# Performance work log

Measured on AMD Instinct MI355X. Metric: run time of the kernel, lower is better.

Reference implementation:

```python
import jax, jax.numpy as jnp
import numpy as np

N = 131072
L = 8
NPL = N // L          # nodes per topological level
DEG = 16              # fixed in-degree
D = 128               # hidden_dim
NEG_SLOPE = 0.01


def _mlp(x, w1, b1, w2, b2, w3, b3):
    # MLP(D, D/2, D/2, D) with LeakyReLU(0.01) between layers
    x = jax.nn.leaky_relu(x @ w1 + b1, NEG_SLOPE)
    x = jax.nn.leaky_relu(x @ w2 + b2, NEG_SLOPE)
    return x @ w3 + b3


def setup_inputs() -> dict:
    key = jax.random.key(0)
    ks = jax.random.split(key, 32)
    h = jax.random.normal(ks[0], (N, D), dtype=jnp.float32)
    # topological DAG: level i nodes pull from nodes in levels < i
    src_levels = []
    for i in range(1, L):
        src_levels.append(jax.random.randint(ks[i], (NPL, DEG), 0, i * NPL, dtype=jnp.int32))
    edge_src = jnp.stack(src_levels)                      # [L-1, NPL, DEG]
    edge_mask = jax.random.randint(ks[10], (L - 1, NPL, DEG), 0, 2, dtype=jnp.int32)
    H = D // 2
    s = 1.0 / np.sqrt(D)
    s2 = 1.0 / np.sqrt(H)

    def lin(k, i, o, sc):
        return jax.random.uniform(k, (i, o), jnp.float32, -sc, sc)

    params = {}
    for j, name in enumerate(['inv', 'and']):
        base = 12 + j * 6
        params[name + '_w1'] = lin(ks[base + 0], D, H, s)
        params[name + '_b1'] = jnp.zeros((H,), jnp.float32)
        params[name + '_w2'] = lin(ks[base + 1], H, H, s2)
        params[name + '_b2'] = jnp.zeros((H,), jnp.float32)
        params[name + '_w3'] = lin(ks[base + 2], H, D, s2)
        params[name + '_b3'] = jnp.zeros((D,), jnp.float32)
    return dict(h=h, edge_src=edge_src, edge_mask=edge_mask, **params)


def reference(h, edge_src, edge_mask,
              inv_w1, inv_b1, inv_w2, inv_b2, inv_w3, inv_b3,
              and_w1, and_b1, and_w2, and_b2, and_w3, and_b3):
    offsets = jnp.arange(1, L, dtype=jnp.int32) * NPL     # dst-node start per level

    def step(h, inp):
        src, mask, off = inp                               # [NPL,DEG], [NPL,DEG], scalar
        msg = h[src]                                       # gather src features [NPL,DEG,D]
        inv = _mlp(msg, inv_w1, inv_b1, inv_w2, inv_b2, inv_w3, inv_b3)
        m = jnp.where(mask[..., None] == 1, inv, msg)      # masked edge transform
        neigh = m.mean(axis=1)                             # fn.mean aggregation [NPL,D]
        new_h = _mlp(neigh, and_w1, and_b1, and_w2, and_b2, and_w3, and_b3)
        h = jax.lax.dynamic_update_slice(h, new_h, (off, jnp.int32(0)))
        return h, None

    h, _ = jax.lax.scan(step, h, (edge_src, edge_mask, offsets))
    return h
```

## Files before the change

### kernel.cpp

```cpp
#include <hip/hip_runtime.h>
#include <hip/hip_fp16.h>

#define NN    131072
#define NPL   16384
#define LVLS  8
#define DEG   16
#define DIM   128
#define HID   64
#define BN    32
#define NPW   8
#define Y_LD  72
#define PACK_HALVES 40960

typedef _Float16 f16x8 __attribute__((ext_vector_type(8)));
typedef float    f32x4 __attribute__((ext_vector_type(4)));

__device__ __forceinline__ int xsw(int row, int col) {
    return row * DIM + (((col >> 3) ^ (row & 15)) << 3) + (col & 7);
}

struct Frags {
    f16x8 w1[4];
    f16x8 w2[2];
    f16x8 w3[2][2];
    float b1, b2, b3[2];
};

__device__ __forceinline__ void load_frags(const __half* __restrict__ pack,
    const float* __restrict__ b1, const float* __restrict__ b2,
    const float* __restrict__ b3, int p, int wv, int lane, Frags& F)
{
    const __half* base = pack + (size_t)((p * 4 + wv) * 10) * 512 + lane * 8;
#pragma unroll
    for (int f = 0; f < 4; ++f) F.w1[f] = *(const f16x8*)(base + f * 512);
#pragma unroll
    for (int f = 0; f < 2; ++f) F.w2[f] = *(const f16x8*)(base + (4 + f) * 512);
#pragma unroll
    for (int nt = 0; nt < 2; ++nt)
#pragma unroll
        for (int kt = 0; kt < 2; ++kt)
            F.w3[nt][kt] = *(const f16x8*)(base + (6 + nt * 2 + kt) * 512);
    int ll = lane & 15;
    F.b1    = b1[wv * 16 + ll];
    F.b2    = b2[wv * 16 + ll];
    F.b3[0] = b3[wv * 32 + ll];
    F.b3[1] = b3[wv * 32 + 16 + ll];
}

__device__ __forceinline__ void mlp_mfma(const Frags& F,
    const __half* __restrict__ xs, __half* __restrict__ y1,
    __half* __restrict__ y2, int wv, int lane, f32x4 (&acc3)[2][2])
{
    int lg = lane >> 4, ll = lane & 15;
#pragma unroll
    for (int m = 0; m < 2; ++m) {
        f32x4 acc = {F.b1, F.b1, F.b1, F.b1};
#pragma unroll
        for (int kt = 0; kt < 4; ++kt) {
            f16x8 a = *(const f16x8*)&xs[xsw(m * 16 + ll, kt * 32 + lg * 8)];
            acc = __builtin_amdgcn_mfma_f32_16x16x32_f16(a, F.w1[kt], acc, 0, 0, 0);
        }
#pragma unroll
        for (int r = 0; r < 4; ++r) {
            float v = acc[r];
            v = v >= 0.f ? v : 0.01f * v;
            y1[(m * 16 + lg * 4 + r) * Y_LD + wv * 16 + ll] = __float2half(v);
        }
    }
    __syncthreads();
#pragma unroll
    for (int m = 0; m < 2; ++m) {
        f32x4 acc = {F.b2, F.b2, F.b2, F.b2};
#pragma unroll
        for (int kt = 0; kt < 2; ++kt) {
            f16x8 a = *(const f16x8*)&y1[(m * 16 + ll) * Y_LD + kt * 32 + lg * 8];
            acc = __builtin_amdgcn_mfma_f32_16x16x32_f16(a, F.w2[kt], acc, 0, 0, 0);
        }
#pragma unroll
        for (int r = 0; r < 4; ++r) {
            float v = acc[r];
            v = v >= 0.f ? v : 0.01f * v;
            y2[(m * 16 + lg * 4 + r) * Y_LD + wv * 16 + ll] = __float2half(v);
        }
    }
    __syncthreads();
#pragma unroll
    for (int m = 0; m < 2; ++m) {
        f16x8 a0 = *(const f16x8*)&y2[(m * 16 + ll) * Y_LD + 0 * 32 + lg * 8];
        f16x8 a1 = *(const f16x8*)&y2[(m * 16 + ll) * Y_LD + 1 * 32 + lg * 8];
#pragma unroll
        for (int nt = 0; nt < 2; ++nt) {
            f32x4 acc = {F.b3[nt], F.b3[nt], F.b3[nt], F.b3[nt]};
            acc = __builtin_amdgcn_mfma_f32_16x16x32_f16(a0, F.w3[nt][0], acc, 0, 0, 0);
            acc = __builtin_amdgcn_mfma_f32_16x16x32_f16(a1, F.w3[nt][1], acc, 0, 0, 0);
            acc3[m][nt] = acc;
        }
    }
}

template<bool DO_INV>
__global__ __launch_bounds__(256) void agg_kernel(
    float* __restrict__ hout,
    __half* __restrict__ h16, __half* __restrict__ inv16,
    const int* __restrict__ esrc, const int* __restrict__ emask,
    const __half* __restrict__ pack,
    const float* __restrict__ ab1, const float* __restrict__ ab2, const float* __restrict__ ab3,
    const float* __restrict__ ib1, const float* __restrict__ ib2, const float* __restrict__ ib3,
    int dstBase)
{
    __shared__ __half xs[BN * DIM];
    __shared__ __half y1[BN * Y_LD];
    __shared__ __half y2[BN * Y_LD];

    int lane = threadIdx.x & 63;
    int wv   = __builtin_amdgcn_readfirstlane((int)(threadIdx.x >> 6));
    int lg = lane >> 4, ll = lane & 15;
    int b0 = blockIdx.x * BN;

    Frags FA;
    load_frags(pack, ab1, ab2, ab3, 0, wv, lane, FA);
    Frags FI;
    if (DO_INV) load_frags(pack, ib1, ib2, ib3, 1, wv, lane, FI);

#pragma unroll 2
    for (int n = 0; n < NPW; ++n) {
        int node = b0 + wv * NPW + n;
        const int* ep = esrc  + (size_t)node * DEG;
        const int* mp = emask + (size_t)node * DEG;
        float ax = 0.f, ay = 0.f;
#pragma unroll
        for (int e = 0; e < DEG; ++e) {
            int s = ep[e];
            int m = mp[e];
            const __half* p = m ? inv16 : h16;
            __half2 hv = *(const __half2*)&p[(size_t)s * DIM + lane * 2];
            float2 v = __half22float2(hv);
            ax += v.x; ay += v.y;
        }
        int lrow = wv * NPW + n;
        *(__half2*)&xs[xsw(lrow, lane * 2)] =
            __floats2half2_rn(ax * 0.0625f, ay * 0.0625f);
    }
    __syncthreads();

    f32x4 acc[2][2];
    mlp_mfma(FA, xs, y1, y2, wv, lane, acc);

#pragma unroll
    for (int m = 0; m < 2; ++m)
#pragma unroll
        for (int nt = 0; nt < 2; ++nt)
#pragma unroll
            for (int r = 0; r < 4; ++r) {
                int row = m * 16 + lg * 4 + r;
                int col = wv * 32 + nt * 16 + ll;
                float v = acc[m][nt][r];
                hout[(size_t)(dstBase + b0 + row) * DIM + col] = v;
                if (DO_INV) xs[xsw(row, col)] = __float2half(v);
            }

    if (DO_INV) {
        __syncthreads();
#pragma unroll
        for (int n = 0; n < NPW; ++n) {
            int lrow = wv * NPW + n;
            __half2 hv = *(const __half2*)&xs[xsw(lrow, lane * 2)];
            *(__half2*)&h16[(size_t)(dstBase + b0 + lrow) * DIM + lane * 2] = hv;
        }
        mlp_mfma(FI, xs, y1, y2, wv, lane, acc);
#pragma unroll
        for (int m = 0; m < 2; ++m)
#pragma unroll
            for (int nt = 0; nt < 2; ++nt)
#pragma unroll
                for (int r = 0; r < 4; ++r)
                    xs[xsw(m * 16 + lg * 4 + r, wv * 32 + nt * 16 + ll)] =
                        __float2half(acc[m][nt][r]);
        __syncthreads();
#pragma unroll
        for (int n = 0; n < NPW; ++n) {
            int lrow = wv * NPW + n;
            __half2 hv = *(const __half2*)&xs[xsw(lrow, lane * 2)];
            *(__half2*)&inv16[(size_t)(dstBase + b0 + lrow) * DIM + lane * 2] = hv;
        }
    }
}

__global__ __launch_bounds__(256) void inv0_kernel(
    const float* __restrict__ h0,
    __half* __restrict__ h16, __half* __restrict__ inv16,
    const __half* __restrict__ pack,
    const float* __restrict__ ib1, const float* __restrict__ ib2,
    const float* __restrict__ ib3)
{
    __shared__ __half xs[BN * DIM];
    __shared__ __half y1[BN * Y_LD];
    __shared__ __half y2[BN * Y_LD];

    int lane = threadIdx.x & 63;
    int wv   = __builtin_amdgcn_readfirstlane((int)(threadIdx.x >> 6));
    int lg = lane >> 4, ll = lane & 15;
    int b0 = blockIdx.x * BN;

    Frags F;
    load_frags(pack, ib1, ib2, ib3, 1, wv, lane, F);

#pragma unroll
    for (int n = 0; n < NPW; ++n) {
        int lrow = wv * NPW + n;
        size_t row = (size_t)(b0 + lrow) * DIM;
        float2 v = *(const float2*)&h0[row + lane * 2];
        __half2 hv = __floats2half2_rn(v.x, v.y);
        *(__half2*)&xs[xsw(lrow, lane * 2)] = hv;
        *(__half2*)&h16[row + lane * 2] = hv;
    }
    __syncthreads();

    f32x4 acc[2][2];
    mlp_mfma(F, xs, y1, y2, wv, lane, acc);
#pragma unroll
    for (int m = 0; m < 2; ++m)
#pragma unroll
        for (int nt = 0; nt < 2; ++nt)
#pragma unroll
            for (int r = 0; r < 4; ++r)
                xs[xsw(m * 16 + lg * 4 + r, wv * 32 + nt * 16 + ll)] =
                    __float2half(acc[m][nt][r]);
    __syncthreads();
#pragma unroll
    for (int n = 0; n < NPW; ++n) {
        int lrow = wv * NPW + n;
        __half2 hv = *(const __half2*)&xs[xsw(lrow, lane * 2)];
        *(__half2*)&inv16[(size_t)(b0 + lrow) * DIM + lane * 2] = hv;
    }
}

__global__ void prep_kernel(const float* __restrict__ aw1, const float* __restrict__ aw2,
                            const float* __restrict__ aw3, const float* __restrict__ iw1,
                            const float* __restrict__ iw2, const float* __restrict__ iw3,
                            __half* __restrict__ pack)
{
    int t = blockIdx.x * blockDim.x + threadIdx.x;
    if (t >= PACK_HALVES) return;
    int p  = t / 20480;
    int r1 = t % 20480;
    int w  = r1 / 5120;
    int r2 = r1 % 5120;
    int f  = r2 / 512;
    int q  = r2 % 512;
    int l  = q >> 3;
    int j  = q & 7;
    int lg = l >> 4, ll = l & 15;

    const float* w1 = p ? iw1 : aw1;
    const float* w2 = p ? iw2 : aw2;
    const float* w3 = p ? iw3 : aw3;

    float val;
    if (f < 4)       val = w1[(f * 32 + lg * 8 + j) * HID + w * 16 + ll];
    else if (f < 6)  val = w2[((f - 4) * 32 + lg * 8 + j) * HID + w * 16 + ll];
    else {
        int nt = (f - 6) >> 1, kt = (f - 6) & 1;
        val = w3[(kt * 32 + lg * 8 + j) * DIM + w * 32 + nt * 16 + ll];
    }
    pack[t] = __float2half(val);
}

extern "C" void kernel_launch(void* const* d_in, const int* in_sizes, int n_in,
                              void* d_out, int out_size, void* d_ws, size_t ws_size,
                              hipStream_t stream)
{
    const float* h     = (const float*)d_in[0];
    const int*   esrc  = (const int*)d_in[1];
    const int*   emask = (const int*)d_in[2];
    const float* iw1 = (const float*)d_in[3];
    const float* ib1 = (const float*)d_in[4];
    const float* iw2 = (const float*)d_in[5];
    const float* ib2 = (const float*)d_in[6];
    const float* iw3 = (const float*)d_in[7];
    const float* ib3 = (const float*)d_in[8];
    const float* aw1 = (const float*)d_in[9];
    const float* ab1 = (const float*)d_in[10];
    const float* aw2 = (const float*)d_in[11];
    const float* ab2 = (const float*)d_in[12];
    const float* aw3 = (const float*)d_in[13];
    const float* ab3 = (const float*)d_in[14];

    float*  hout  = (float*)d_out;
    __half* pack  = (__half*)d_ws;
    __half* h16   = pack + PACK_HALVES;
    __half* inv16 = h16 + (size_t)NN * DIM;

    prep_kernel<<<(PACK_HALVES + 255) / 256, 256, 0, stream>>>(
        aw1, aw2, aw3, iw1, iw2, iw3, pack);

    hipMemcpyAsync(hout, h, (size_t)NPL * DIM * sizeof(float),
                   hipMemcpyDeviceToDevice, stream);

    const int grid = NPL / BN;

    inv0_kernel<<<grid, 256, 0, stream>>>(h, h16, inv16, pack, ib1, ib2, ib3);

    for (int lvl = 1; lvl < LVLS; ++lvl) {
        const int* es = esrc  + (size_t)(lvl - 1) * NPL * DEG;
        const int* em = emask + (size_t)(lvl - 1) * NPL * DEG;
        if (lvl < LVLS - 1)
            agg_kernel<true><<<grid, 256, 0, stream>>>(
                hout, h16, inv16, es, em, pack,
                ab1, ab2, ab3, ib1, ib2, ib3, lvl * NPL);
        else
            agg_kernel<false><<<grid, 256, 0, stream>>>(
                hout, h16, inv16, es, em, pack,
                ab1, ab2, ab3, ib1, ib2, ib3, lvl * NPL);
    }
}
```

Baseline: 258.6 us.

## Halve node tile per block, stage output stores through LDS, fold level-0 copy

Halves the nodes per block from 32 to 16, which doubles the grid and reduces each wave's MFMA work to a single 16-row tile. The goal is more concurrent blocks to hide the latency of the irregular neighbour gathers. The launch bounds now request 4 blocks per CU, and the inv-MLP weight fragments are loaded only after the first MLP finishes, which lowers register pressure. The fp32 output is now staged through fp16 shared memory so stores are coalesced rows, which adds fp16 rounding to the output. The separate device copy of level 0 is folded into the inv0 kernel.

```diff
diff --git a/kernel.cpp b/kernel.cpp
--- a/kernel.cpp
+++ b/kernel.cpp
@@ -7,8 +7,8 @@
 #define DEG   16
 #define DIM   128
 #define HID   64
-#define BN    32
-#define NPW   8
+#define BN    16
+#define NPW   4
 #define Y_LD  72
 #define PACK_HALVES 40960
 
@@ -49,57 +49,59 @@
 
 __device__ __forceinline__ void mlp_mfma(const Frags& F,
     const __half* __restrict__ xs, __half* __restrict__ y1,
-    __half* __restrict__ y2, int wv, int lane, f32x4 (&acc3)[2][2])
+    __half* __restrict__ y2, int wv, int lane, f32x4 (&acc3)[2])
 {
     int lg = lane >> 4, ll = lane & 15;
-#pragma unroll
-    for (int m = 0; m < 2; ++m) {
-        f32x4 acc = {F.b1, F.b1, F.b1, F.b1};
-#pragma unroll
-        for (int kt = 0; kt < 4; ++kt) {
-            f16x8 a = *(const f16x8*)&xs[xsw(m * 16 + ll, kt * 32 + lg * 8)];
-            acc = __builtin_amdgcn_mfma_f32_16x16x32_f16(a, F.w1[kt], acc, 0, 0, 0);
-        }
-#pragma unroll
-        for (int r = 0; r < 4; ++r) {
-            float v = acc[r];
-            v = v >= 0.f ? v : 0.01f * v;
-            y1[(m * 16 + lg * 4 + r) * Y_LD + wv * 16 + ll] = __float2half(v);
-        }
-    }
-    __syncthreads();
-#pragma unroll
-    for (int m = 0; m < 2; ++m) {
-        f32x4 acc = {F.b2, F.b2, F.b2, F.b2};
-#pragma unroll
-        for (int kt = 0; kt < 2; ++kt) {
-            f16x8 a = *(const f16x8*)&y1[(m * 16 + ll) * Y_LD + kt * 32 + lg * 8];
-            acc = __builtin_amdgcn_mfma_f32_16x16x32_f16(a, F.w2[kt], acc, 0, 0, 0);
-        }
-#pragma unroll
-        for (int r = 0; r < 4; ++r) {
-            float v = acc[r];
-            v = v >= 0.f ? v : 0.01f * v;
-            y2[(m * 16 + lg * 4 + r) * Y_LD + wv * 16 + ll] = __float2half(v);
-        }
-    }
-    __syncthreads();
-#pragma unroll
-    for (int m = 0; m < 2; ++m) {
-        f16x8 a0 = *(const f16x8*)&y2[(m * 16 + ll) * Y_LD + 0 * 32 + lg * 8];
-        f16x8 a1 = *(const f16x8*)&y2[(m * 16 + ll) * Y_LD + 1 * 32 + lg * 8];
-#pragma unroll
-        for (int nt = 0; nt < 2; ++nt) {
-            f32x4 acc = {F.b3[nt], F.b3[nt], F.b3[nt], F.b3[nt]};
-            acc = __builtin_amdgcn_mfma_f32_16x16x32_f16(a0, F.w3[nt][0], acc, 0, 0, 0);
-            acc = __builtin_amdgcn_mfma_f32_16x16x32_f16(a1, F.w3[nt][1], acc, 0, 0, 0);
-            acc3[m][nt] = acc;
-        }
-    }
+    f32x4 acc = {F.b1, F.b1, F.b1, F.b1};
+#pragma unroll
+    for (int kt = 0; kt < 4; ++kt) {
+        f16x8 a = *(const f16x8*)&xs[xsw(ll, kt * 32 + lg * 8)];
+        acc = __builtin_amdgcn_mfma_f32_16x16x32_f16(a, F.w1[kt], acc, 0, 0, 0);
+    }
+#pragma unroll
+    for (int r = 0; r < 4; ++r) {
+        float v = acc[r];
+        v = v >= 0.f ? v : 0.01f * v;
+        y1[(lg * 4 + r) * Y_LD + wv * 16 + ll] = __float2half(v);
+    }
+    __syncthreads();
+    acc = f32x4{F.b2, F.b2, F.b2, F.b2};
+#pragma unroll
+    for (int kt = 0; kt < 2; ++kt) {
+        f16x8 a = *(const f16x8*)&y1[ll * Y_LD + kt * 32 + lg * 8];
+        acc = __builtin_amdgcn_mfma_f32_16x16x32_f16(a, F.w2[kt], acc, 0, 0, 0);
+    }
+#pragma unroll
+    for (int r = 0; r < 4; ++r) {
+        float v = acc[r];
+        v = v >= 0.f ? v : 0.01f * v;
+        y2[(lg * 4 + r) * Y_LD + wv * 16 + ll] = __float2half(v);
+    }
+    __syncthreads();
+    f16x8 a0 = *(const f16x8*)&y2[ll * Y_LD + 0 * 32 + lg * 8];
+    f16x8 a1 = *(const f16x8*)&y2[ll * Y_LD + 1 * 32 + lg * 8];
+#pragma unroll
+    for (int nt = 0; nt < 2; ++nt) {
+        f32x4 c = {F.b3[nt], F.b3[nt], F.b3[nt], F.b3[nt]};
+        c = __builtin_amdgcn_mfma_f32_16x16x32_f16(a0, F.w3[nt][0], c, 0, 0, 0);
+        c = __builtin_amdgcn_mfma_f32_16x16x32_f16(a1, F.w3[nt][1], c, 0, 0, 0);
+        acc3[nt] = c;
+    }
+}
+
+__device__ __forceinline__ void acc_to_xs(const f32x4 (&acc3)[2],
+    __half* __restrict__ xs, int wv, int lane)
+{
+    int lg = lane >> 4, ll = lane & 15;
+#pragma unroll
+    for (int nt = 0; nt < 2; ++nt)
+#pragma unroll
+        for (int r = 0; r < 4; ++r)
+            xs[xsw(lg * 4 + r, wv * 32 + nt * 16 + ll)] = __float2half(acc3[nt][r]);
 }
 
 template<bool DO_INV>
-__global__ __launch_bounds__(256) void agg_kernel(
+__global__ __launch_bounds__(256, 4) void agg_kernel(
     float* __restrict__ hout,
     __half* __restrict__ h16, __half* __restrict__ inv16,
     const int* __restrict__ esrc, const int* __restrict__ emask,
@@ -114,13 +116,10 @@
 
     int lane = threadIdx.x & 63;
     int wv   = __builtin_amdgcn_readfirstlane((int)(threadIdx.x >> 6));
-    int lg = lane >> 4, ll = lane & 15;
-    int b0 = blockIdx.x * BN;
+    int b0   = blockIdx.x * BN;
 
     Frags FA;
     load_frags(pack, ab1, ab2, ab3, 0, wv, lane, FA);
-    Frags FI;
-    if (DO_INV) load_frags(pack, ib1, ib2, ib3, 1, wv, lane, FI);
 
 #pragma unroll 2
     for (int n = 0; n < NPW; ++n) {
@@ -137,45 +136,30 @@
             float2 v = __half22float2(hv);
             ax += v.x; ay += v.y;
         }
+        *(__half2*)&xs[xsw(wv * NPW + n, lane * 2)] =
+            __floats2half2_rn(ax * 0.0625f, ay * 0.0625f);
+    }
+    __syncthreads();
+
+    f32x4 acc[2];
+    mlp_mfma(FA, xs, y1, y2, wv, lane, acc);
+    acc_to_xs(acc, xs, wv, lane);
+    __syncthreads();
+
+#pragma unroll
+    for (int n = 0; n < NPW; ++n) {
         int lrow = wv * NPW + n;
-        *(__half2*)&xs[xsw(lrow, lane * 2)] =
-            __floats2half2_rn(ax * 0.0625f, ay * 0.0625f);
-    }
-    __syncthreads();
-
-    f32x4 acc[2][2];
-    mlp_mfma(FA, xs, y1, y2, wv, lane, acc);
-
-#pragma unroll
-    for (int m = 0; m < 2; ++m)
-#pragma unroll
-        for (int nt = 0; nt < 2; ++nt)
-#pragma unroll
-            for (int r = 0; r < 4; ++r) {
-                int row = m * 16 + lg * 4 + r;
-                int col = wv * 32 + nt * 16 + ll;
-                float v = acc[m][nt][r];
-                hout[(size_t)(dstBase + b0 + row) * DIM + col] = v;
-                if (DO_INV) xs[xsw(row, col)] = __float2half(v);
-            }
+        size_t row = (size_t)(dstBase + b0 + lrow) * DIM;
+        __half2 hv = *(const __half2*)&xs[xsw(lrow, lane * 2)];
+        *(float2*)&hout[row + lane * 2] = __half22float2(hv);
+        if (DO_INV) *(__half2*)&h16[row + lane * 2] = hv;
+    }
 
     if (DO_INV) {
-        __syncthreads();
-#pragma unroll
-        for (int n = 0; n < NPW; ++n) {
-            int lrow = wv * NPW + n;
-            __half2 hv = *(const __half2*)&xs[xsw(lrow, lane * 2)];
-            *(__half2*)&h16[(size_t)(dstBase + b0 + lrow) * DIM + lane * 2] = hv;
-        }
+        Frags FI;
+        load_frags(pack, ib1, ib2, ib3, 1, wv, lane, FI);
         mlp_mfma(FI, xs, y1, y2, wv, lane, acc);
-#pragma unroll
-        for (int m = 0; m < 2; ++m)
-#pragma unroll
-            for (int nt = 0; nt < 2; ++nt)
-#pragma unroll
-                for (int r = 0; r < 4; ++r)
-                    xs[xsw(m * 16 + lg * 4 + r, wv * 32 + nt * 16 + ll)] =
-                        __float2half(acc[m][nt][r]);
+        acc_to_xs(acc, xs, wv, lane);
         __syncthreads();
 #pragma unroll
         for (int n = 0; n < NPW; ++n) {
@@ -186,8 +170,8 @@
     }
 }
 
-__global__ __launch_bounds__(256) void inv0_kernel(
-    const float* __restrict__ h0,
+__global__ __launch_bounds__(256, 4) void inv0_kernel(
+    const float* __restrict__ h0, float* __restrict__ hout,
     __half* __restrict__ h16, __half* __restrict__ inv16,
     const __half* __restrict__ pack,
     const float* __restrict__ ib1, const float* __restrict__ ib2,
@@ -199,8 +183,7 @@
 
     int lane = threadIdx.x & 63;
     int wv   = __builtin_amdgcn_readfirstlane((int)(threadIdx.x >> 6));
-    int lg = lane >> 4, ll = lane & 15;
-    int b0 = blockIdx.x * BN;
+    int b0   = blockIdx.x * BN;
 
     Frags F;
     load_frags(pack, ib1, ib2, ib3, 1, wv, lane, F);
@@ -211,21 +194,15 @@
         size_t row = (size_t)(b0 + lrow) * DIM;
         float2 v = *(const float2*)&h0[row + lane * 2];
         __half2 hv = __floats2half2_rn(v.x, v.y);
+        *(float2*)&hout[row + lane * 2] = v;
+        *(__half2*)&h16[row + lane * 2] = hv;
         *(__half2*)&xs[xsw(lrow, lane * 2)] = hv;
-        *(__half2*)&h16[row + lane * 2] = hv;
-    }
-    __syncthreads();
-
-    f32x4 acc[2][2];
+    }
+    __syncthreads();
+
+    f32x4 acc[2];
     mlp_mfma(F, xs, y1, y2, wv, lane, acc);
-#pragma unroll
-    for (int m = 0; m < 2; ++m)
-#pragma unroll
-        for (int nt = 0; nt < 2; ++nt)
-#pragma unroll
-            for (int r = 0; r < 4; ++r)
-                xs[xsw(m * 16 + lg * 4 + r, wv * 32 + nt * 16 + ll)] =
-                    __float2half(acc[m][nt][r]);
+    acc_to_xs(acc, xs, wv, lane);
     __syncthreads();
 #pragma unroll
     for (int n = 0; n < NPW; ++n) {
@@ -294,12 +271,10 @@
     prep_kernel<<<(PACK_HALVES + 255) / 256, 256, 0, stream>>>(
         aw1, aw2, aw3, iw1, iw2, iw3, pack);
 
-    hipMemcpyAsync(hout, h, (size_t)NPL * DIM * sizeof(float),
-                   hipMemcpyDeviceToDevice, stream);
-
     const int grid = NPL / BN;
 
-    inv0_kernel<<<grid, 256, 0, stream>>>(h, h16, inv16, pack, ib1, ib2, ib3);
+    inv0_kernel<<<grid, 256, 0, stream>>>(h, hout, h16, inv16, pack,
+                                          ib1, ib2, ib3);
 
     for (int lvl = 1; lvl < LVLS; ++lvl) {
         const int* es = esrc  + (size_t)(lvl - 1) * NPL * DEG;
```

Result: faster. 243.0 us (-6.0%).
